# Kernel tuning notes

Measured on AMD Instinct MI355X. Metric: run time of the kernel, lower is better.

## Reference

```python
import jax, jax.numpy as jnp
import numpy as np

BS, SEQ, C, NC, H, W = 8, 512, 512, 5, 768, 768


def setup_inputs() -> dict:
    key = jax.random.key(0)
    k1, k2, k3, k4, k5, k6, k7, k8 = jax.random.split(key, 8)
    fuse_embeddings = jax.random.normal(k1, (BS, SEQ, C), dtype=jnp.float32)
    class_labels = jax.random.normal(k2, (BS, NC, H, W), dtype=jnp.float32)
    # valid boxes: x0<x1<=W, y0<y1<=H (coords order: x0, y0, x1, y1)
    x0 = jax.random.randint(k3, (BS, SEQ), 0, W - 1)
    y0 = jax.random.randint(k4, (BS, SEQ), 0, H - 1)
    x1 = jnp.minimum(x0 + jax.random.randint(k5, (BS, SEQ), 1, 64), W)
    y1 = jnp.minimum(y0 + jax.random.randint(k6, (BS, SEQ), 1, 16), H)
    coords = jnp.stack([x0, y0, x1, y1], axis=-1).astype(jnp.int32)
    mask = jax.random.randint(k7, (BS, SEQ), 0, 2).astype(jnp.int32)
    # classification_net (Linear) params
    bound = 1.0 / np.sqrt(C)
    Wc = jax.random.uniform(k8, (NC, C), minval=-bound, maxval=bound, dtype=jnp.float32)
    bc = jnp.zeros((NC,), dtype=jnp.float32)
    return {"fuse_embeddings": fuse_embeddings, "class_labels": class_labels,
            "Wc": Wc, "bc": bc, "coords": coords, "mask": mask}


def _forward(fuse_embeddings, class_labels, Wc, bc, coords, mask):
    bs, seq_len, _ = fuse_embeddings.shape
    nc = Wc.shape[0]
    # linear classifier over all tokens: [bs, seq, nc]
    logits = jnp.einsum("bsc,nc->bsn", fuse_embeddings, Wc) + bc
    # per-pixel hard label: [bs, H, W]
    lab = jnp.argmax(class_labels, axis=1)
    onehot = jax.nn.one_hot(lab, nc, dtype=logits.dtype)  # [bs, H, W, nc]
    # padded integral image -> O(1) box histograms (replaces per-ROI bincount)
    ii = jnp.cumsum(jnp.cumsum(onehot, axis=1), axis=2)
    ii = jnp.pad(ii, ((0, 0), (1, 0), (1, 0), (0, 0)))  # [bs, H+1, W+1, nc]
    x0, y0, x1, y1 = coords[..., 0], coords[..., 1], coords[..., 2], coords[..., 3]
    # degenerate-box fix from the original code
    y1 = jnp.where(y1 == y0, y1 + 1, y1)
    x1 = jnp.where(x1 == x0, x1 + 1, x1)
    b_idx = jnp.arange(bs)[:, None]
    g = lambda y, x: ii[b_idx, y, x, :]
    counts = g(y1, x1) - g(y0, x1) - g(y1, x0) + g(y0, x0)  # [bs, seq, nc]
    maj = jnp.argmax(counts, axis=-1)  # majority-vote label, first-max tiebreak like bincount().argmax()
    # masked-mean cross entropy (CE over tokens with mask==1)
    logp = jax.nn.log_softmax(logits, axis=-1)
    nll = -jnp.take_along_axis(logp, maj[..., None], axis=-1)[..., 0]
    m = (mask == 1).astype(logits.dtype)
    return jnp.sum(nll * m) / jnp.sum(m)


def reference(fuse_embeddings, class_labels, Wc, bc, coords, mask):
    return _forward(fuse_embeddings, class_labels, Wc, bc, coords, mask)
```

## Files before the change

kernel.cpp:

```cpp
#include <hip/hip_runtime.h>

#define BS 8
#define SEQ 512
#define CDIM 512
#define NC 5
#define IMG_H 768
#define IMG_W 768
#define HW (IMG_H * IMG_W)
#define NTOK (BS * SEQ)
#define NBLK (NTOK / 4)

__global__ __launch_bounds__(256) void token_kernel(
    const float* __restrict__ emb,
    const float* __restrict__ cls,
    const float* __restrict__ Wc,
    const float* __restrict__ bc,
    const int*   __restrict__ coords,
    const int*   __restrict__ mask,
    float2* __restrict__ ws)
{
    const int t     = threadIdx.x;
    const int wave  = t >> 6;
    const int lane  = t & 63;
    const int token = blockIdx.x * 4 + wave;
    const int b     = token >> 9;

    int x0 = coords[token * 4 + 0];
    int y0 = coords[token * 4 + 1];
    int x1 = coords[token * 4 + 2];
    int y1 = coords[token * 4 + 3];
    if (y1 == y0) y1++;
    if (x1 == x0) x1++;
    if (x1 > IMG_W) x1 = IMG_W;
    if (y1 > IMG_H) y1 = IMG_H;

    unsigned long long hp = 0ull;
    {
        const int xx = x0 + lane;
        const bool xok = (xx < x1);
        const float* p0 = cls + (size_t)b * NC * HW + y0 * IMG_W + xx;
#pragma unroll 4
        for (int yy = y0; yy < y1; ++yy, p0 += IMG_W) {
            if (xok) {
                const float v0 = p0[0 * HW];
                const float v1 = p0[1 * HW];
                const float v2 = p0[2 * HW];
                const float v3 = p0[3 * HW];
                const float v4 = p0[4 * HW];
                int lab = 0; float best = v0;
                if (v1 > best) { best = v1; lab = 1; }
                if (v2 > best) { best = v2; lab = 2; }
                if (v3 > best) { best = v3; lab = 3; }
                if (v4 > best) { best = v4; lab = 4; }
                hp += 1ull << (lab * 12);
            }
        }
    }

    const float* e = emb + (size_t)token * CDIM + lane * 8;
    const float4 e0 = *(const float4*)(e);
    const float4 e1 = *(const float4*)(e + 4);
    float part[NC];
#pragma unroll
    for (int c = 0; c < NC; ++c) {
        const float* w = Wc + c * CDIM + lane * 8;
        const float4 w0 = *(const float4*)(w);
        const float4 w1 = *(const float4*)(w + 4);
        part[c] = e0.x * w0.x + e0.y * w0.y + e0.z * w0.z + e0.w * w0.w
                + e1.x * w1.x + e1.y * w1.y + e1.z * w1.z + e1.w * w1.w;
    }

#pragma unroll
    for (int off = 32; off >= 1; off >>= 1) {
#pragma unroll
        for (int c = 0; c < NC; ++c) part[c] += __shfl_down(part[c], off);
        hp += __shfl_down(hp, off);
    }

    __shared__ float2 s_pair[4];
    if (lane == 0) {
        float l[NC];
#pragma unroll
        for (int c = 0; c < NC; ++c) l[c] = part[c] + bc[c];

        int maj = 0;
        int bestc = (int)(hp & 4095);
#pragma unroll
        for (int c = 1; c < NC; ++c) {
            const int hc = (int)((hp >> (12 * c)) & 4095);
            if (hc > bestc) { bestc = hc; maj = c; }
        }

        float m = l[0];
#pragma unroll
        for (int c = 1; c < NC; ++c) m = fmaxf(m, l[c]);
        float s = 0.0f;
#pragma unroll
        for (int c = 0; c < NC; ++c) s += __expf(l[c] - m);
        const float nll = m + __logf(s) - l[maj];

        const float mk = (mask[token] == 1) ? 1.0f : 0.0f;
        s_pair[wave] = make_float2(nll * mk, mk);
    }
    __syncthreads();

    if (t == 0) {
        const float2 a = s_pair[0], b2 = s_pair[1],
                     c2 = s_pair[2], d2 = s_pair[3];
        ws[blockIdx.x] = make_float2(a.x + b2.x + c2.x + d2.x,
                                     a.y + b2.y + c2.y + d2.y);
    }
}

__global__ __launch_bounds__(256) void finalize_kernel(
    const float2* __restrict__ ws, float* __restrict__ out)
{
    float a = 0.0f, bsum = 0.0f;
#pragma unroll
    for (int i = threadIdx.x; i < NBLK; i += 256) {
        const float2 v = ws[i];
        a += v.x; bsum += v.y;
    }
#pragma unroll
    for (int off = 32; off >= 1; off >>= 1) {
        a    += __shfl_down(a, off);
        bsum += __shfl_down(bsum, off);
    }
    __shared__ float sa[4], sb[4];
    const int wave = threadIdx.x >> 6;
    if ((threadIdx.x & 63) == 0) { sa[wave] = a; sb[wave] = bsum; }
    __syncthreads();
    if (threadIdx.x == 0) {
        a    = sa[0] + sa[1] + sa[2] + sa[3];
        bsum = sb[0] + sb[1] + sb[2] + sb[3];
        out[0] = a / bsum;
    }
}

extern "C" void kernel_launch(void* const* d_in, const int* in_sizes, int n_in,
                              void* d_out, int out_size, void* d_ws, size_t ws_size,
                              hipStream_t stream) {
    const float* emb    = (const float*)d_in[0];
    const float* cls    = (const float*)d_in[1];
    const float* Wc     = (const float*)d_in[2];
    const float* bc     = (const float*)d_in[3];
    const int*   coords = (const int*)d_in[4];
    const int*   mask   = (const int*)d_in[5];
    float* out = (float*)d_out;
    float2* ws = (float2*)d_ws;

    token_kernel<<<NBLK, 256, 0, stream>>>(emb, cls, Wc, bc, coords, mask, ws);
    finalize_kernel<<<1, 256, 0, stream>>>(ws, out);
}
```

Baseline: 147.3 us.

## Precompute per-pixel argmax label map only for box-covered tiles, then histogram bytes

```diff
diff --git a/kernel.cpp b/kernel.cpp
--- a/kernel.cpp
+++ b/kernel.cpp
@@ -9,15 +9,108 @@
 #define HW (IMG_H * IMG_W)
 #define NTOK (BS * SEQ)
 #define NBLK (NTOK / 4)
+#define NROWS (BS * IMG_H)
+#define TILE 32
+
+#define WS_MASK_OFF     0
+#define WS_CNT_OFF      24576
+#define WS_PART_OFF     32768
+#define WS_MAP_OFF      65536
+
+__device__ __forceinline__ void fix_box(int& x0, int& y0, int& x1, int& y1) {
+    if (y1 == y0) y1++;
+    if (x1 == x0) x1++;
+    if (x1 > IMG_W) x1 = IMG_W;
+    if (y1 > IMG_H) y1 = IMG_H;
+}
+
+__global__ __launch_bounds__(256) void mask_kernel(
+    const int* __restrict__ coords, unsigned int* __restrict__ rowmask)
+{
+    const int idx   = blockIdx.x * 256 + threadIdx.x;
+    const int token = idx >> 4;
+    const int r     = idx & 15;
+    int x0 = coords[token * 4 + 0];
+    int y0 = coords[token * 4 + 1];
+    int x1 = coords[token * 4 + 2];
+    int y1 = coords[token * 4 + 3];
+    fix_box(x0, y0, x1, y1);
+    const int yy = y0 + r;
+    if (yy < y1) {
+        const int t0 = x0 >> 5;
+        const int t1 = (x1 - 1) >> 5;
+        const unsigned int bits = ((1u << (t1 - t0 + 1)) - 1u) << t0;
+        const int b = token >> 9;
+        atomicOr(&rowmask[b * IMG_H + yy], bits);
+    }
+}
+
+__global__ __launch_bounds__(256) void map_kernel(
+    const float* __restrict__ cls,
+    const unsigned int* __restrict__ rowmask,
+    unsigned char* __restrict__ map)
+{
+    const int wave = threadIdx.x >> 6;
+    const int lane = threadIdx.x & 63;
+    const int w    = blockIdx.x * 4 + wave;
+    const int b    = w / IMG_H;
+    const int y    = w - b * IMG_H;
+
+    unsigned int m = rowmask[w];
+    const float*         rowp = cls + (size_t)b * NC * HW + y * IMG_W;
+    unsigned char*       mrow = map + (size_t)(b * IMG_H + y) * IMG_W;
+    const int j = lane >> 3;
+    const int i = lane & 7;
+
+    while (m) {
+        int tile = -1;
+        {
+            unsigned int mm = m;
+            int need = j;
+            while (mm) {
+                const int bpos = __ffs(mm) - 1;
+                if (need == 0) { tile = bpos; break; }
+                mm &= mm - 1; --need;
+            }
+        }
+        if (tile >= 0) {
+            const int px = tile * TILE + i * 4;
+            const float4 v0 = *(const float4*)(rowp + px + 0 * HW);
+            const float4 v1 = *(const float4*)(rowp + px + 1 * HW);
+            const float4 v2 = *(const float4*)(rowp + px + 2 * HW);
+            const float4 v3 = *(const float4*)(rowp + px + 3 * HW);
+            const float4 v4 = *(const float4*)(rowp + px + 4 * HW);
+            auto amax = [](float c0, float c1, float c2, float c3, float c4)
+                -> unsigned char {
+                int lab = 0; float best = c0;
+                if (c1 > best) { best = c1; lab = 1; }
+                if (c2 > best) { best = c2; lab = 2; }
+                if (c3 > best) { best = c3; lab = 3; }
+                if (c4 > best) { best = c4; lab = 4; }
+                return (unsigned char)lab;
+            };
+            uchar4 out;
+            out.x = amax(v0.x, v1.x, v2.x, v3.x, v4.x);
+            out.y = amax(v0.y, v1.y, v2.y, v3.y, v4.y);
+            out.z = amax(v0.z, v1.z, v2.z, v3.z, v4.z);
+            out.w = amax(v0.w, v1.w, v2.w, v3.w, v4.w);
+            *(uchar4*)(mrow + px) = out;
+        }
+#pragma unroll
+        for (int k = 0; k < 8; ++k) m &= (m - 1);
+    }
+}
 
 __global__ __launch_bounds__(256) void token_kernel(
     const float* __restrict__ emb,
-    const float* __restrict__ cls,
+    const unsigned char* __restrict__ map,
     const float* __restrict__ Wc,
     const float* __restrict__ bc,
     const int*   __restrict__ coords,
     const int*   __restrict__ mask,
-    float2* __restrict__ ws)
+    float2* __restrict__ partials,
+    unsigned int* __restrict__ counter,
+    float* __restrict__ out)
 {
     const int t     = threadIdx.x;
     const int wave  = t >> 6;
@@ -29,31 +122,16 @@
     int y0 = coords[token * 4 + 1];
     int x1 = coords[token * 4 + 2];
     int y1 = coords[token * 4 + 3];
-    if (y1 == y0) y1++;
-    if (x1 == x0) x1++;
-    if (x1 > IMG_W) x1 = IMG_W;
-    if (y1 > IMG_H) y1 = IMG_H;
+    fix_box(x0, y0, x1, y1);
 
     unsigned long long hp = 0ull;
     {
         const int xx = x0 + lane;
-        const bool xok = (xx < x1);
-        const float* p0 = cls + (size_t)b * NC * HW + y0 * IMG_W + xx;
-#pragma unroll 4
-        for (int yy = y0; yy < y1; ++yy, p0 += IMG_W) {
-            if (xok) {
-                const float v0 = p0[0 * HW];
-                const float v1 = p0[1 * HW];
-                const float v2 = p0[2 * HW];
-                const float v3 = p0[3 * HW];
-                const float v4 = p0[4 * HW];
-                int lab = 0; float best = v0;
-                if (v1 > best) { best = v1; lab = 1; }
-                if (v2 > best) { best = v2; lab = 2; }
-                if (v3 > best) { best = v3; lab = 3; }
-                if (v4 > best) { best = v4; lab = 4; }
-                hp += 1ull << (lab * 12);
-            }
+        if (xx < x1) {
+            const unsigned char* p =
+                map + (size_t)(b * IMG_H + y0) * IMG_W + xx;
+            for (int yy = y0; yy < y1; ++yy, p += IMG_W)
+                hp += 1ull << ((int)(*p) * 12);
         }
     }
 
@@ -78,6 +156,7 @@
     }
 
     __shared__ float2 s_pair[4];
+    __shared__ int s_last;
     if (lane == 0) {
         float l[NC];
 #pragma unroll
@@ -90,7 +169,6 @@
             const int hc = (int)((hp >> (12 * c)) & 4095);
             if (hc > bestc) { bestc = hc; maj = c; }
         }
-
         float m = l[0];
 #pragma unroll
         for (int c = 1; c < NC; ++c) m = fmaxf(m, l[c]);
@@ -98,7 +176,6 @@
 #pragma unroll
         for (int c = 0; c < NC; ++c) s += __expf(l[c] - m);
         const float nll = m + __logf(s) - l[maj];
-
         const float mk = (mask[token] == 1) ? 1.0f : 0.0f;
         s_pair[wave] = make_float2(nll * mk, mk);
     }
@@ -107,33 +184,34 @@
     if (t == 0) {
         const float2 a = s_pair[0], b2 = s_pair[1],
                      c2 = s_pair[2], d2 = s_pair[3];
-        ws[blockIdx.x] = make_float2(a.x + b2.x + c2.x + d2.x,
-                                     a.y + b2.y + c2.y + d2.y);
-    }
-}
-
-__global__ __launch_bounds__(256) void finalize_kernel(
-    const float2* __restrict__ ws, float* __restrict__ out)
-{
-    float a = 0.0f, bsum = 0.0f;
-#pragma unroll
-    for (int i = threadIdx.x; i < NBLK; i += 256) {
-        const float2 v = ws[i];
-        a += v.x; bsum += v.y;
-    }
-#pragma unroll
-    for (int off = 32; off >= 1; off >>= 1) {
-        a    += __shfl_down(a, off);
-        bsum += __shfl_down(bsum, off);
-    }
-    __shared__ float sa[4], sb[4];
-    const int wave = threadIdx.x >> 6;
-    if ((threadIdx.x & 63) == 0) { sa[wave] = a; sb[wave] = bsum; }
+        partials[blockIdx.x] = make_float2(a.x + b2.x + c2.x + d2.x,
+                                           a.y + b2.y + c2.y + d2.y);
+        __threadfence();
+        s_last = (atomicAdd(counter, 1u) == NBLK - 1);
+    }
     __syncthreads();
-    if (threadIdx.x == 0) {
-        a    = sa[0] + sa[1] + sa[2] + sa[3];
-        bsum = sb[0] + sb[1] + sb[2] + sb[3];
-        out[0] = a / bsum;
+
+    if (s_last) {
+        __threadfence();
+        float a = 0.0f, bsum = 0.0f;
+#pragma unroll
+        for (int i = t; i < NBLK; i += 256) {
+            const float2 v = partials[i];
+            a += v.x; bsum += v.y;
+        }
+#pragma unroll
+        for (int off = 32; off >= 1; off >>= 1) {
+            a    += __shfl_down(a, off);
+            bsum += __shfl_down(bsum, off);
+        }
+        __shared__ float sa[4], sb[4];
+        if (lane == 0) { sa[wave] = a; sb[wave] = bsum; }
+        __syncthreads();
+        if (t == 0) {
+            a    = sa[0] + sa[1] + sa[2] + sa[3];
+            bsum = sb[0] + sb[1] + sb[2] + sb[3];
+            out[0] = a / bsum;
+        }
     }
 }
 
@@ -147,8 +225,16 @@
     const int*   coords = (const int*)d_in[4];
     const int*   mask   = (const int*)d_in[5];
     float* out = (float*)d_out;
-    float2* ws = (float2*)d_ws;
-
-    token_kernel<<<NBLK, 256, 0, stream>>>(emb, cls, Wc, bc, coords, mask, ws);
-    finalize_kernel<<<1, 256, 0, stream>>>(ws, out);
-}
+
+    char* ws = (char*)d_ws;
+    unsigned int*  rowmask  = (unsigned int*)(ws + WS_MASK_OFF);
+    unsigned int*  counter  = (unsigned int*)(ws + WS_CNT_OFF);
+    float2*        partials = (float2*)(ws + WS_PART_OFF);
+    unsigned char* map      = (unsigned char*)(ws + WS_MAP_OFF);
+
+    hipMemsetAsync(ws, 0, WS_CNT_OFF + 4, stream);
+    mask_kernel<<<(NTOK * 16) / 256, 256, 0, stream>>>(coords, rowmask);
+    map_kernel<<<NROWS / 4, 256, 0, stream>>>(cls, rowmask, map);
+    token_kernel<<<NBLK, 256, 0, stream>>>(emb, map, Wc, bc, coords, mask,
+                                           partials, counter, out);
+}
```

Result: slower. 185.9 us (+26.2%).

## Precompute byte label map in a streaming pass and fuse final reduction

Applied to the files above, without the earlier changes.

```diff
diff --git a/kernel.cpp b/kernel.cpp
--- a/kernel.cpp
+++ b/kernel.cpp
@@ -10,14 +10,63 @@
 #define NTOK (BS * SEQ)
 #define NBLK (NTOK / 4)
 
+#define WS_CNT_OFF      0
+#define WS_PART_OFF     4096
+#define WS_MAP_OFF      65536
+
+__device__ __forceinline__ void fix_box(int& x0, int& y0, int& x1, int& y1) {
+    if (y1 == y0) y1++;
+    if (x1 == x0) x1++;
+    if (x1 > IMG_W) x1 = IMG_W;
+    if (y1 > IMG_H) y1 = IMG_H;
+}
+
+__global__ __launch_bounds__(256) void map_kernel(
+    const float* __restrict__ cls,
+    unsigned char* __restrict__ map,
+    unsigned int* __restrict__ counter)
+{
+    if (blockIdx.x == 0 && threadIdx.x == 0) *counter = 0u;
+
+    const int g  = blockIdx.x * 256 + threadIdx.x;
+    const int px = g * 4;
+    const int b  = px / HW;
+    const int o  = px - b * HW;
+
+    const float* p = cls + (size_t)b * NC * HW + o;
+    const float4 v0 = *(const float4*)(p + 0 * HW);
+    const float4 v1 = *(const float4*)(p + 1 * HW);
+    const float4 v2 = *(const float4*)(p + 2 * HW);
+    const float4 v3 = *(const float4*)(p + 3 * HW);
+    const float4 v4 = *(const float4*)(p + 4 * HW);
+
+    auto amax = [](float c0, float c1, float c2, float c3, float c4)
+        -> unsigned char {
+        int lab = 0; float best = c0;
+        if (c1 > best) { best = c1; lab = 1; }
+        if (c2 > best) { best = c2; lab = 2; }
+        if (c3 > best) { best = c3; lab = 3; }
+        if (c4 > best) { best = c4; lab = 4; }
+        return (unsigned char)lab;
+    };
+    uchar4 outv;
+    outv.x = amax(v0.x, v1.x, v2.x, v3.x, v4.x);
+    outv.y = amax(v0.y, v1.y, v2.y, v3.y, v4.y);
+    outv.z = amax(v0.z, v1.z, v2.z, v3.z, v4.z);
+    outv.w = amax(v0.w, v1.w, v2.w, v3.w, v4.w);
+    *(uchar4*)(map + (size_t)b * HW + o) = outv;
+}
+
 __global__ __launch_bounds__(256) void token_kernel(
     const float* __restrict__ emb,
-    const float* __restrict__ cls,
+    const unsigned char* __restrict__ map,
     const float* __restrict__ Wc,
     const float* __restrict__ bc,
     const int*   __restrict__ coords,
     const int*   __restrict__ mask,
-    float2* __restrict__ ws)
+    float2* __restrict__ partials,
+    unsigned int* __restrict__ counter,
+    float* __restrict__ out)
 {
     const int t     = threadIdx.x;
     const int wave  = t >> 6;
@@ -29,31 +78,16 @@
     int y0 = coords[token * 4 + 1];
     int x1 = coords[token * 4 + 2];
     int y1 = coords[token * 4 + 3];
-    if (y1 == y0) y1++;
-    if (x1 == x0) x1++;
-    if (x1 > IMG_W) x1 = IMG_W;
-    if (y1 > IMG_H) y1 = IMG_H;
+    fix_box(x0, y0, x1, y1);
 
     unsigned long long hp = 0ull;
     {
         const int xx = x0 + lane;
-        const bool xok = (xx < x1);
-        const float* p0 = cls + (size_t)b * NC * HW + y0 * IMG_W + xx;
-#pragma unroll 4
-        for (int yy = y0; yy < y1; ++yy, p0 += IMG_W) {
-            if (xok) {
-                const float v0 = p0[0 * HW];
-                const float v1 = p0[1 * HW];
-                const float v2 = p0[2 * HW];
-                const float v3 = p0[3 * HW];
-                const float v4 = p0[4 * HW];
-                int lab = 0; float best = v0;
-                if (v1 > best) { best = v1; lab = 1; }
-                if (v2 > best) { best = v2; lab = 2; }
-                if (v3 > best) { best = v3; lab = 3; }
-                if (v4 > best) { best = v4; lab = 4; }
-                hp += 1ull << (lab * 12);
-            }
+        if (xx < x1) {
+            const unsigned char* p =
+                map + (size_t)(b * IMG_H + y0) * IMG_W + xx;
+            for (int yy = y0; yy < y1; ++yy, p += IMG_W)
+                hp += 1ull << ((int)(*p) * 12);
         }
     }
 
@@ -78,6 +112,7 @@
     }
 
     __shared__ float2 s_pair[4];
+    __shared__ int s_last;
     if (lane == 0) {
         float l[NC];
 #pragma unroll
@@ -90,7 +125,6 @@
             const int hc = (int)((hp >> (12 * c)) & 4095);
             if (hc > bestc) { bestc = hc; maj = c; }
         }
-
         float m = l[0];
 #pragma unroll
         for (int c = 1; c < NC; ++c) m = fmaxf(m, l[c]);
@@ -98,7 +132,6 @@
 #pragma unroll
         for (int c = 0; c < NC; ++c) s += __expf(l[c] - m);
         const float nll = m + __logf(s) - l[maj];
-
         const float mk = (mask[token] == 1) ? 1.0f : 0.0f;
         s_pair[wave] = make_float2(nll * mk, mk);
     }
@@ -107,33 +140,34 @@
     if (t == 0) {
         const float2 a = s_pair[0], b2 = s_pair[1],
                      c2 = s_pair[2], d2 = s_pair[3];
-        ws[blockIdx.x] = make_float2(a.x + b2.x + c2.x + d2.x,
-                                     a.y + b2.y + c2.y + d2.y);
+        partials[blockIdx.x] = make_float2(a.x + b2.x + c2.x + d2.x,
+                                           a.y + b2.y + c2.y + d2.y);
+        __threadfence();
+        s_last = (atomicAdd(counter, 1u) == NBLK - 1);
     }
-}
+    __syncthreads();
 
-__global__ __launch_bounds__(256) void finalize_kernel(
-    const float2* __restrict__ ws, float* __restrict__ out)
-{
-    float a = 0.0f, bsum = 0.0f;
+    if (s_last) {
+        __threadfence();
+        float a = 0.0f, bsum = 0.0f;
 #pragma unroll
-    for (int i = threadIdx.x; i < NBLK; i += 256) {
-        const float2 v = ws[i];
-        a += v.x; bsum += v.y;
-    }
+        for (int i = t; i < NBLK; i += 256) {
+            const float2 v = partials[i];
+            a += v.x; bsum += v.y;
+        }
 #pragma unroll
-    for (int off = 32; off >= 1; off >>= 1) {
-        a    += __shfl_down(a, off);
-        bsum += __shfl_down(bsum, off);
-    }
-    __shared__ float sa[4], sb[4];
-    const int wave = threadIdx.x >> 6;
-    if ((threadIdx.x & 63) == 0) { sa[wave] = a; sb[wave] = bsum; }
-    __syncthreads();
-    if (threadIdx.x == 0) {
-        a    = sa[0] + sa[1] + sa[2] + sa[3];
-        bsum = sb[0] + sb[1] + sb[2] + sb[3];
-        out[0] = a / bsum;
+        for (int off = 32; off >= 1; off >>= 1) {
+            a    += __shfl_down(a, off);
+            bsum += __shfl_down(bsum, off);
+        }
+        __shared__ float sa[4], sb[4];
+        if (lane == 0) { sa[wave] = a; sb[wave] = bsum; }
+        __syncthreads();
+        if (t == 0) {
+            a    = sa[0] + sa[1] + sa[2] + sa[3];
+            bsum = sb[0] + sb[1] + sb[2] + sb[3];
+            out[0] = a / bsum;
+        }
     }
 }
 
@@ -147,8 +181,13 @@
     const int*   coords = (const int*)d_in[4];
     const int*   mask   = (const int*)d_in[5];
     float* out = (float*)d_out;
-    float2* ws = (float2*)d_ws;
 
-    token_kernel<<<NBLK, 256, 0, stream>>>(emb, cls, Wc, bc, coords, mask, ws);
-    finalize_kernel<<<1, 256, 0, stream>>>(ws, out);
+    char* ws = (char*)d_ws;
+    unsigned int*  counter  = (unsigned int*)(ws + WS_CNT_OFF);
+    float2*        partials = (float2*)(ws + WS_PART_OFF);
+    unsigned char* map      = (unsigned char*)(ws + WS_MAP_OFF);
+
+    map_kernel<<<(BS * HW) / 1024, 256, 0, stream>>>(cls, map, counter);
+    token_kernel<<<NBLK, 256, 0, stream>>>(emb, map, Wc, bc, coords, mask,
+                                           partials, counter, out);
 }
```

After: 182.6 us. 24.0% more time.
